# Optimization experiments

Measured on AMD Instinct MI355X. Metric: run time of the kernel, lower is better.

Reference implementation:

```python
import jax, jax.numpy as jnp
import numpy as np
import itertools

EPS = 1e-5
SCALE = 16 ** -0.5  # key_dim ** -0.5
H_HEADS, KEY_DIM, D, RES, RES_, STRIDE = 8, 16, 32, 28, 14, 2


def hardswish(x):
    return x * jnp.clip(x + 3.0, 0.0, 6.0) / 6.0


def conv_bn_hw(x, w, g, b, m, v):
    # 1x1 conv (no bias) + eval-mode BatchNorm + Hardswish
    y = jnp.einsum('bchw,oc->bohw', x, w)
    scale = (g / jnp.sqrt(v + EPS))[:, None, None]
    y = (y - m[:, None, None]) * scale + b[:, None, None]
    return hardswish(y)


def _bias_idxs():
    offsets, idxs = {}, []
    for p1 in itertools.product(range(RES_), repeat=2):
        for p2 in itertools.product(range(RES), repeat=2):
            off = (abs(p1[0] * STRIDE - p2[0]), abs(p1[1] * STRIDE - p2[1]))
            if off not in offsets:
                offsets[off] = len(offsets)
            idxs.append(offsets[off])
    return np.array(idxs, dtype=np.int32).reshape(RES_ * RES_, RES * RES), len(offsets)


def setup_inputs() -> dict:
    key = jax.random.key(0)
    ks = jax.random.split(key, 8)
    B, C = 64, 256
    idxs, n_off = _bias_idxs()

    def bn_params(k, n):
        k1, k2, k3, k4 = jax.random.split(k, 4)
        return (jax.random.normal(k1, (n,)) * 0.1 + 1.0,
                jax.random.normal(k2, (n,)) * 0.1,
                jax.random.normal(k3, (n,)) * 0.1,
                jax.random.uniform(k4, (n,), minval=0.5, maxval=1.5))

    kv_g, kv_b, kv_m, kv_v = bn_params(ks[1], 384)
    q_g, q_b, q_m, q_v = bn_params(ks[2], 128)
    p_g, p_b, p_m, p_v = bn_params(ks[3], 512)
    return dict(
        x=jax.random.normal(ks[0], (B, C, 28, 28), dtype=jnp.float32),
        kv_w=jax.random.normal(ks[4], (384, C)) * 0.05,
        kv_g=kv_g, kv_b=kv_b, kv_m=kv_m, kv_v=kv_v,
        q_w=jax.random.normal(ks[5], (128, C)) * 0.05,
        q_g=q_g, q_b=q_b, q_m=q_m, q_v=q_v,
        proj_w=jax.random.normal(ks[6], (512, 256)) * 0.05,
        proj_g=p_g, proj_b=p_b, proj_m=p_m, proj_v=p_v,
        ab=jax.random.normal(ks[7], (H_HEADS, n_off)) * 0.02,
        bias_idxs=jnp.asarray(idxs),
    )


def reference(x, kv_w, kv_g, kv_b, kv_m, kv_v, q_w, q_g, q_b, q_m, q_v,
              proj_w, proj_g, proj_b, proj_m, proj_v, ab, bias_idxs):
    B = x.shape[0]
    N, N_ = RES * RES, RES_ * RES_
    kv = conv_bn_hw(x, kv_w, kv_g, kv_b, kv_m, kv_v).reshape(B, H_HEADS, KEY_DIM + D, N)
    k, v = kv[:, :, :KEY_DIM], kv[:, :, KEY_DIM:]
    # AvgPool2d(kernel=1, stride=2) == strided slice
    q = conv_bn_hw(x[:, :, ::STRIDE, ::STRIDE], q_w, q_g, q_b, q_m, q_v)
    q = q.reshape(B, H_HEADS, KEY_DIM, N_)
    bias = ab[:, bias_idxs]  # gather -> [H, N_, N]
    attn = jax.nn.softmax(jnp.einsum('bhdn,bhdm->bhnm', q, k) * SCALE + bias, axis=-1)
    out = jnp.einsum('bhdm,bhnm->bhdn', v, attn).reshape(B, H_HEADS * D, RES_, RES_)
    return conv_bn_hw(hardswish(out), proj_w, proj_g, proj_b, proj_m, proj_v)
```

## Files before the change

### kernel.cpp

```cpp
#include <hip/hip_runtime.h>
#include <cstddef>


#define SCALE_ATTN 0.25f
#define BN_EPS 1e-5f

typedef short s8v  __attribute__((ext_vector_type(8)));
typedef short s4v  __attribute__((ext_vector_type(4)));
typedef float f4v  __attribute__((ext_vector_type(4)));

__device__ __forceinline__ float hswish(float y) {
    float t = fminf(fmaxf(y + 3.0f, 0.0f), 6.0f);
    return y * t * (1.0f / 6.0f);
}

__device__ __forceinline__ unsigned short bf16_rn(float f) {
    unsigned u = __float_as_uint(f);
    unsigned r = (u + 0x7FFFu + ((u >> 16) & 1u)) >> 16;
    return (unsigned short)r;
}
__device__ __forceinline__ float bf16_to_f(unsigned short h) {
    return __uint_as_float(((unsigned)h) << 16);
}

__global__ __launch_bounds__(256)
void bias_kernel(const float* __restrict__ ab, const int* __restrict__ idxs,
                 unsigned short* __restrict__ biasB, int n_off)
{
    __shared__ int I[32][33];
    int mx = blockIdx.x * 32, ny = blockIdx.y * 32;
    int tx = threadIdx.x & 31, ty = threadIdx.x >> 5;
#pragma unroll
    for (int i = 0; i < 4; ++i) {
        int nl = ty + i * 8;
        int n = ny + nl, m = mx + tx;
        I[tx][nl] = (n < 196 && m < 784) ? idxs[n * 784 + m] : 0;
    }
    __syncthreads();
#pragma unroll
    for (int i = 0; i < 4; ++i) {
        int ml = ty + i * 8;
        int m = mx + ml, n = ny + tx;
        if (m < 784 && n < 208) {
            float v = 0.0f;
            if (n < 196) {
                int id = I[ml][tx];
#pragma unroll
                for (int h = 0; h < 8; ++h) {
                    biasB[((size_t)h * 784 + m) * 208 + n] = bf16_rn(ab[h * n_off + id]);
                }
            } else {
#pragma unroll
                for (int h = 0; h < 8; ++h) {
                    biasB[((size_t)h * 784 + m) * 208 + n] = 0;
                }
            }
            (void)v;
        }
    }
}

template<bool STRIDED>
__global__ __launch_bounds__(256)
void convbn_mfma(const float* __restrict__ X, const float* __restrict__ W,
                 const float* __restrict__ G, const float* __restrict__ Bb,
                 const float* __restrict__ Mm, const float* __restrict__ Vv,
                 float* __restrict__ Y, int O, int N, int xbstride, int HWsrc)
{
    __shared__ short Ah[64][72];
    __shared__ short Al[64][72];
    __shared__ short Bh[64][72];
    __shared__ short Bl[64][72];
    __shared__ float scs[64], shs[64];

    const int C = 256;
    int b = blockIdx.z;
    int oBase = blockIdx.y * 64;
    int nBase = blockIdx.x * 64;
    const float* Xb = X + (size_t)b * xbstride;
    int tid = threadIdx.x;
    int w = tid >> 6, l = tid & 63;
    int wm = w >> 1, wn = w & 1;

    if (tid < 64) {
        int o = oBase + tid;
        float sc = G[o] * rsqrtf(Vv[o] + BN_EPS);
        scs[tid] = sc;
        shs[tid] = Bb[o] - Mm[o] * sc;
    }

    f4v acc[2][2];
#pragma unroll
    for (int i = 0; i < 2; ++i)
#pragma unroll
        for (int j = 0; j < 2; ++j) acc[i][j] = (f4v)0.0f;

    int sr  = tid >> 4;
    int sc4 = (tid & 15) * 4;
    int fr = l & 15, fk = (l >> 4) * 8;

    for (int c0 = 0; c0 < C; c0 += 64) {
        __syncthreads();
#pragma unroll
        for (int jo = 0; jo < 4; ++jo) {
            int o = sr + jo * 16;
            float4 wv = *reinterpret_cast<const float4*>(
                &W[(size_t)(oBase + o) * C + c0 + sc4]);
            s4v hv, lv;
            {
                unsigned short h;
                h = bf16_rn(wv.x); hv[0] = (short)h; lv[0] = (short)bf16_rn(wv.x - bf16_to_f(h));
                h = bf16_rn(wv.y); hv[1] = (short)h; lv[1] = (short)bf16_rn(wv.y - bf16_to_f(h));
                h = bf16_rn(wv.z); hv[2] = (short)h; lv[2] = (short)bf16_rn(wv.z - bf16_to_f(h));
                h = bf16_rn(wv.w); hv[3] = (short)h; lv[3] = (short)bf16_rn(wv.w - bf16_to_f(h));
            }
            *reinterpret_cast<s4v*>(&Ah[o][sc4]) = hv;
            *reinterpret_cast<s4v*>(&Al[o][sc4]) = lv;
        }
#pragma unroll
        for (int jc = 0; jc < 4; ++jc) {
            int c = sr + jc * 16;
            float vals[4];
            if (!STRIDED) {
                if (nBase + sc4 + 3 < N) {
                    float4 xv = *reinterpret_cast<const float4*>(
                        &Xb[(size_t)(c0 + c) * HWsrc + nBase + sc4]);
                    vals[0] = xv.x; vals[1] = xv.y; vals[2] = xv.z; vals[3] = xv.w;
                } else {
#pragma unroll
                    for (int e = 0; e < 4; ++e) {
                        int nn = nBase + sc4 + e;
                        vals[e] = (nn < N) ? Xb[(size_t)(c0 + c) * HWsrc + nn] : 0.0f;
                    }
                }
            } else {
#pragma unroll
                for (int e = 0; e < 4; ++e) {
                    int nn = nBase + sc4 + e;
                    float vv = 0.0f;
                    if (nn < N) {
                        int r = nn / 14, cc = nn - r * 14;
                        vv = Xb[(size_t)(c0 + c) * HWsrc + r * 56 + cc * 2];
                    }
                    vals[e] = vv;
                }
            }
#pragma unroll
            for (int e = 0; e < 4; ++e) {
                unsigned short h = bf16_rn(vals[e]);
                Bh[sc4 + e][c] = (short)h;
                Bl[sc4 + e][c] = (short)bf16_rn(vals[e] - bf16_to_f(h));
            }
        }
        __syncthreads();
#pragma unroll
        for (int ks = 0; ks < 2; ++ks) {
            s8v aH[2], aL[2], bH[2], bL[2];
#pragma unroll
            for (int mf = 0; mf < 2; ++mf) {
                aH[mf] = *reinterpret_cast<const s8v*>(&Ah[wm * 32 + mf * 16 + fr][ks * 32 + fk]);
                aL[mf] = *reinterpret_cast<const s8v*>(&Al[wm * 32 + mf * 16 + fr][ks * 32 + fk]);
            }
#pragma unroll
            for (int nf = 0; nf < 2; ++nf) {
                bH[nf] = *reinterpret_cast<const s8v*>(&Bh[wn * 32 + nf * 16 + fr][ks * 32 + fk]);
                bL[nf] = *reinterpret_cast<const s8v*>(&Bl[wn * 32 + nf * 16 + fr][ks * 32 + fk]);
            }
#pragma unroll
            for (int mf = 0; mf < 2; ++mf)
#pragma unroll
                for (int nf = 0; nf < 2; ++nf) {
                    acc[mf][nf] = __builtin_amdgcn_mfma_f32_16x16x32_bf16(aH[mf], bH[nf], acc[mf][nf], 0, 0, 0);
                    acc[mf][nf] = __builtin_amdgcn_mfma_f32_16x16x32_bf16(aH[mf], bL[nf], acc[mf][nf], 0, 0, 0);
                    acc[mf][nf] = __builtin_amdgcn_mfma_f32_16x16x32_bf16(aL[mf], bH[nf], acc[mf][nf], 0, 0, 0);
                }
        }
    }

    int lr = l >> 4;
#pragma unroll
    for (int mf = 0; mf < 2; ++mf)
#pragma unroll
        for (int nf = 0; nf < 2; ++nf) {
            int n = nBase + wn * 32 + nf * 16 + fr;
            if (n < N) {
#pragma unroll
                for (int i = 0; i < 4; ++i) {
                    int ol = wm * 32 + mf * 16 + lr * 4 + i;
                    float v = acc[mf][nf][i] * scs[ol] + shs[ol];
                    Y[((size_t)b * O + oBase + ol) * N + n] = hswish(v);
                }
            }
        }
}

__global__ __launch_bounds__(256)
void attn_mfma(const float* __restrict__ kv, const float* __restrict__ q,
               const unsigned short* __restrict__ biasB, float* __restrict__ act)
{
    __shared__ short Kh[64][24];
    __shared__ short Kl[64][24];
    __shared__ short Vs[32][72];
    __shared__ unsigned short Bia[64][208];
    __shared__ short Pl[4][16][72];

    int bh = blockIdx.x;
    int b = bh >> 3, h = bh & 7;
    const float* kvb = kv + ((size_t)b * 384 + h * 48) * 784;
    const float* qb  = q  + ((size_t)b * 128 + h * 16) * 196;
    const unsigned short* bB = biasB + (size_t)h * 784 * 208;

    int tid = threadIdx.x;
    int w = tid >> 6, l = tid & 63;
    int g = l >> 4, fr = l & 15;

    s8v qh[4], ql[4];
#pragma unroll
    for (int i = 0; i < 4; ++i) { qh[i] = (s8v)0; ql[i] = (s8v)0; }
#pragma unroll
    for (int i = 0; i < 4; ++i) {
        int tile = i * 4 + w;
        if (tile < 13 && g < 2) {
            int n = tile * 16 + fr;
            if (n < 196) {
#pragma unroll
                for (int j = 0; j < 8; ++j) {
                    int d = g * 8 + j;
                    float qv = qb[(size_t)d * 196 + n];
                    unsigned short hh = bf16_rn(qv);
                    qh[i][j] = (short)hh;
                    ql[i][j] = (short)bf16_rn(qv - bf16_to_f(hh));
                }
            }
        }
    }

    f4v Oa[4][2];
    float M[4], L[4];
#pragma unroll
    for (int i = 0; i < 4; ++i) {
        Oa[i][0] = (f4v)0.0f; Oa[i][1] = (f4v)0.0f;
        M[i] = -1e30f; L[i] = 0.0f;
    }

#pragma unroll 1
    for (int ch = 0; ch < 13; ++ch) {
        int m0 = ch * 64;
        int mlim = (784 - m0 < 64) ? (784 - m0) : 64;
        __syncthreads();
        {
            int d = tid >> 4, m4 = tid & 15;
            float4 kvv = make_float4(0.f, 0.f, 0.f, 0.f);
            if (m4 * 4 < mlim)
                kvv = *reinterpret_cast<const float4*>(&kvb[(size_t)d * 784 + m0 + m4 * 4]);
            float e0[4] = {kvv.x, kvv.y, kvv.z, kvv.w};
#pragma unroll
            for (int e = 0; e < 4; ++e) {
                unsigned short hh = bf16_rn(e0[e]);
                Kh[m4 * 4 + e][d] = (short)hh;
                Kl[m4 * 4 + e][d] = (short)bf16_rn(e0[e] - bf16_to_f(hh));
            }
        }
        {
            int d = tid >> 3, m8 = (tid & 7) * 8;
            float4 a = make_float4(0.f, 0.f, 0.f, 0.f), c4 = a;
            if (m8 < mlim) {
                a  = *reinterpret_cast<const float4*>(&kvb[(size_t)(16 + d) * 784 + m0 + m8]);
                c4 = *reinterpret_cast<const float4*>(&kvb[(size_t)(16 + d) * 784 + m0 + m8 + 4]);
            }
            s4v v0, v1;
            v0[0] = (short)bf16_rn(a.x);  v0[1] = (short)bf16_rn(a.y);
            v0[2] = (short)bf16_rn(a.z);  v0[3] = (short)bf16_rn(a.w);
            v1[0] = (short)bf16_rn(c4.x); v1[1] = (short)bf16_rn(c4.y);
            v1[2] = (short)bf16_rn(c4.z); v1[3] = (short)bf16_rn(c4.w);
            *reinterpret_cast<s4v*>(&Vs[d][m8])     = v0;
            *reinterpret_cast<s4v*>(&Vs[d][m8 + 4]) = v1;
        }
        {
            for (int it = tid; it < 64 * 26; it += 256) {
                int r = it / 26, cseg = it - r * 26;
                int4 vz = make_int4(0, 0, 0, 0);
                if (r < mlim)
                    vz = *reinterpret_cast<const int4*>(&bB[(size_t)(m0 + r) * 208 + cseg * 8]);
                *reinterpret_cast<int4*>(&Bia[r][cseg * 8]) = vz;
            }
        }
        __syncthreads();

#pragma unroll
        for (int i = 0; i < 4; ++i) {
            int tile = i * 4 + w;
            if (tile >= 13) continue;
            int n = tile * 16 + fr;

            float s[4][4];
#pragma unroll
            for (int sub = 0; sub < 4; ++sub) {
                s8v ah = (s8v)0, al = (s8v)0;
                if (g < 2) {
                    ah = *reinterpret_cast<const s8v*>(&Kh[sub * 16 + fr][g * 8]);
                    al = *reinterpret_cast<const s8v*>(&Kl[sub * 16 + fr][g * 8]);
                }
                f4v acc = (f4v)0.0f;
                acc = __builtin_amdgcn_mfma_f32_16x16x32_bf16(ah, qh[i], acc, 0, 0, 0);
                acc = __builtin_amdgcn_mfma_f32_16x16x32_bf16(ah, ql[i], acc, 0, 0, 0);
                acc = __builtin_amdgcn_mfma_f32_16x16x32_bf16(al, qh[i], acc, 0, 0, 0);
#pragma unroll
                for (int e = 0; e < 4; ++e) {
                    int mm = sub * 16 + g * 4 + e;
                    s[sub][e] = acc[e] * SCALE_ATTN + bf16_to_f(Bia[mm][n]);
                }
            }
            float mx = s[0][0];
#pragma unroll
            for (int sub = 0; sub < 4; ++sub)
#pragma unroll
                for (int e = 0; e < 4; ++e) mx = fmaxf(mx, s[sub][e]);
            mx = fmaxf(mx, __shfl_xor(mx, 16));
            mx = fmaxf(mx, __shfl_xor(mx, 32));
            if (__any(mx > M[i] + 8.0f)) {
                float Mn = fmaxf(M[i], mx);
                float corr = __expf(M[i] - Mn);
                L[i] *= corr;
#pragma unroll
                for (int e = 0; e < 4; ++e) { Oa[i][0][e] *= corr; Oa[i][1][e] *= corr; }
                M[i] = Mn;
            }
            float Ls = 0.0f;
#pragma unroll
            for (int sub = 0; sub < 4; ++sub) {
                float p[4];
#pragma unroll
                for (int e = 0; e < 4; ++e) {
                    int mm = sub * 16 + g * 4 + e;
                    float pv = __expf(s[sub][e] - M[i]);
                    p[e] = (mm < mlim) ? pv : 0.0f;
                    Ls += p[e];
                }
                unsigned w0 = (unsigned)bf16_rn(p[0]) | ((unsigned)bf16_rn(p[1]) << 16);
                unsigned w1 = (unsigned)bf16_rn(p[2]) | ((unsigned)bf16_rn(p[3]) << 16);
                int mbase = sub * 16 + g * 4;
                *reinterpret_cast<unsigned*>(&Pl[w][fr][mbase])     = w0;
                *reinterpret_cast<unsigned*>(&Pl[w][fr][mbase + 2]) = w1;
            }
            Ls += __shfl_xor(Ls, 16);
            Ls += __shfl_xor(Ls, 32);
            L[i] += Ls;
#pragma unroll
            for (int kc = 0; kc < 2; ++kc) {
                s8v pf = *reinterpret_cast<const s8v*>(&Pl[w][fr][kc * 32 + g * 8]);
                s8v v0 = *reinterpret_cast<const s8v*>(&Vs[fr][kc * 32 + g * 8]);
                s8v v1 = *reinterpret_cast<const s8v*>(&Vs[16 + fr][kc * 32 + g * 8]);
                Oa[i][0] = __builtin_amdgcn_mfma_f32_16x16x32_bf16(v0, pf, Oa[i][0], 0, 0, 0);
                Oa[i][1] = __builtin_amdgcn_mfma_f32_16x16x32_bf16(v1, pf, Oa[i][1], 0, 0, 0);
            }
        }
    }

#pragma unroll
    for (int i = 0; i < 4; ++i) {
        int tile = i * 4 + w;
        if (tile >= 13) continue;
        int n = tile * 16 + fr;
        if (n < 196) {
            float inv = 1.0f / L[i];
#pragma unroll
            for (int dt = 0; dt < 2; ++dt)
#pragma unroll
                for (int e = 0; e < 4; ++e) {
                    int d = dt * 16 + g * 4 + e;
                    float z = Oa[i][dt][e] * inv;
                    act[((size_t)b * 256 + h * 32 + d) * 196 + n] = hswish(z);
                }
        }
    }
}

extern "C" void kernel_launch(void* const* d_in, const int* in_sizes, int n_in,
                              void* d_out, int out_size, void* d_ws, size_t ws_size,
                              hipStream_t stream) {
    const float* x      = (const float*)d_in[0];
    const float* kv_w   = (const float*)d_in[1];
    const float* kv_g   = (const float*)d_in[2];
    const float* kv_b   = (const float*)d_in[3];
    const float* kv_m   = (const float*)d_in[4];
    const float* kv_v   = (const float*)d_in[5];
    const float* q_w    = (const float*)d_in[6];
    const float* q_g    = (const float*)d_in[7];
    const float* q_b    = (const float*)d_in[8];
    const float* q_m    = (const float*)d_in[9];
    const float* q_v    = (const float*)d_in[10];
    const float* proj_w = (const float*)d_in[11];
    const float* proj_g = (const float*)d_in[12];
    const float* proj_b = (const float*)d_in[13];
    const float* proj_m = (const float*)d_in[14];
    const float* proj_v = (const float*)d_in[15];
    const float* ab     = (const float*)d_in[16];
    const int*   idxs   = (const int*)d_in[17];
    float* out = (float*)d_out;

    int n_off = in_sizes[16] / 8;

    const size_t KV_ELEMS   = (size_t)64 * 384 * 784;
    const size_t Q_ELEMS    = (size_t)64 * 128 * 196;
    const size_t BIAS_SHORT = (size_t)8 * 784 * 208;
    float* kvbuf = (float*)d_ws;
    float* qbuf  = kvbuf + KV_ELEMS;
    unsigned short* biasB = (unsigned short*)(qbuf + Q_ELEMS);
    float* actb  = (float*)(biasB + BIAS_SHORT);

    {
        dim3 g(25, 7);
        bias_kernel<<<g, 256, 0, stream>>>(ab, idxs, biasB, n_off);
    }
    {
        dim3 g(13, 6, 64);
        convbn_mfma<false><<<g, 256, 0, stream>>>(x, kv_w, kv_g, kv_b, kv_m, kv_v,
                                                  kvbuf, 384, 784, 256 * 784, 784);
    }
    {
        dim3 g(4, 2, 64);
        convbn_mfma<true><<<g, 256, 0, stream>>>(x, q_w, q_g, q_b, q_m, q_v,
                                                 qbuf, 128, 196, 256 * 784, 784);
    }
    {
        attn_mfma<<<512, 256, 0, stream>>>(kvbuf, qbuf, biasB, actb);
    }
    {
        dim3 g(4, 8, 64);
        convbn_mfma<false><<<g, 256, 0, stream>>>(actb, proj_w, proj_g, proj_b, proj_m, proj_v,
                                                  out, 512, 196, 256 * 196, 196);
    }
}
```

Before: 396.9 us.

## Pre-split weights and inputs to bf16 hi/lo, swizzled tiles, restructure GEMMs and attention

Weights are split into bf16 hi/lo once in prep kernels instead of in every GEMM block. The input x is transposed into swizzled bf16 hi/lo tiles that later GEMMs load directly into LDS with global_load_lds. Intermediates K, Q, V and the attention output are now stored in bf16 (hi/lo where needed) in layouts the next stage consumes, which cuts fp32 traffic and per-block conversion work. The GEMMs use a 128-row output tile, and attention is relaunched with 512 threads and a new tile assignment. This adds several extra launches, and V is stored as single bf16, which may change accuracy.

```diff
diff --git a/kernel.cpp b/kernel.cpp
--- a/kernel.cpp
+++ b/kernel.cpp
@@ -1,19 +1,19 @@
 #include <hip/hip_runtime.h>
 #include <cstddef>
+#include <cstdint>
 
 
 #define SCALE_ATTN 0.25f
 #define BN_EPS 1e-5f
 
-typedef short s8v  __attribute__((ext_vector_type(8)));
-typedef short s4v  __attribute__((ext_vector_type(4)));
-typedef float f4v  __attribute__((ext_vector_type(4)));
+typedef short s8v __attribute__((ext_vector_type(8)));
+typedef short s4v __attribute__((ext_vector_type(4)));
+typedef float f4v __attribute__((ext_vector_type(4)));
 
 __device__ __forceinline__ float hswish(float y) {
     float t = fminf(fmaxf(y + 3.0f, 0.0f), 6.0f);
     return y * t * (1.0f / 6.0f);
 }
-
 __device__ __forceinline__ unsigned short bf16_rn(float f) {
     unsigned u = __float_as_uint(f);
     unsigned r = (u + 0x7FFFu + ((u >> 16) & 1u)) >> 16;
@@ -21,6 +21,79 @@
 }
 __device__ __forceinline__ float bf16_to_f(unsigned short h) {
     return __uint_as_float(((unsigned)h) << 16);
+}
+__device__ __forceinline__ void gload_lds16(const void* gsrc, void* ldsdst) {
+    __builtin_amdgcn_global_load_lds(
+        (const __attribute__((address_space(1))) unsigned int*)gsrc,
+        (__attribute__((address_space(3))) unsigned int*)ldsdst, 16, 0, 0);
+}
+
+__global__ __launch_bounds__(256)
+void wprep(const float* __restrict__ W, short* __restrict__ hi,
+           short* __restrict__ lo, int n4)
+{
+    int i = blockIdx.x * 256 + threadIdx.x;
+    int stride = gridDim.x * 256;
+    for (; i < n4; i += stride) {
+        float4 v = reinterpret_cast<const float4*>(W)[i];
+        s4v h, l;
+        unsigned short hh;
+        hh = bf16_rn(v.x); h[0] = (short)hh; l[0] = (short)bf16_rn(v.x - bf16_to_f(hh));
+        hh = bf16_rn(v.y); h[1] = (short)hh; l[1] = (short)bf16_rn(v.y - bf16_to_f(hh));
+        hh = bf16_rn(v.z); h[2] = (short)hh; l[2] = (short)bf16_rn(v.z - bf16_to_f(hh));
+        hh = bf16_rn(v.w); h[3] = (short)hh; l[3] = (short)bf16_rn(v.w - bf16_to_f(hh));
+        reinterpret_cast<s4v*>(hi)[i] = h;
+        reinterpret_cast<s4v*>(lo)[i] = l;
+    }
+}
+
+__global__ __launch_bounds__(256)
+void xprep(const float* __restrict__ x, short* __restrict__ xT)
+{
+    __shared__ float T[64][65];
+    int nt = blockIdx.x, b = blockIdx.y;
+    int n0 = nt * 64;
+    const float* xb = x + (size_t)b * 256 * 784;
+    int t = threadIdx.x;
+    int cr = t >> 2, s = t & 3;
+
+    for (int ct = 0; ct < 4; ++ct) {
+        __syncthreads();
+#pragma unroll
+        for (int qq = 0; qq < 4; ++qq) {
+            int n = n0 + s * 16 + qq * 4;
+            float4 v = make_float4(0.f, 0.f, 0.f, 0.f);
+            if (n + 3 < 784)
+                v = *reinterpret_cast<const float4*>(&xb[(size_t)(ct * 64 + cr) * 784 + n]);
+            *reinterpret_cast<float4*>(&T[cr][s * 16 + qq * 4]) = v;
+        }
+        __syncthreads();
+        int r = cr;
+        if (n0 + r < 784) {
+            size_t tb = ((((size_t)b * 13 + nt) * 4 + ct) << 13);
+            short* hiB = xT + tb;
+            short* loB = xT + tb + 4096;
+            s8v h0, h1, l0, l1;
+#pragma unroll
+            for (int j = 0; j < 8; ++j) {
+                float f = T[s * 16 + j][r];
+                unsigned short hh = bf16_rn(f);
+                h0[j] = (short)hh; l0[j] = (short)bf16_rn(f - bf16_to_f(hh));
+            }
+#pragma unroll
+            for (int j = 0; j < 8; ++j) {
+                float f = T[s * 16 + 8 + j][r];
+                unsigned short hh = bf16_rn(f);
+                h1[j] = (short)hh; l1[j] = (short)bf16_rn(f - bf16_to_f(hh));
+            }
+            int sw = (r & 7) << 3;
+            int base = r * 64;
+            *reinterpret_cast<s8v*>(&hiB[base + ((s * 16) ^ sw)]) = h0;
+            *reinterpret_cast<s8v*>(&hiB[base + ((s * 16 + 8) ^ sw)]) = h1;
+            *reinterpret_cast<s8v*>(&loB[base + ((s * 16) ^ sw)]) = l0;
+            *reinterpret_cast<s8v*>(&loB[base + ((s * 16 + 8) ^ sw)]) = l1;
+        }
+    }
 }
 
 __global__ __launch_bounds__(256)
@@ -42,203 +115,267 @@
         int ml = ty + i * 8;
         int m = mx + ml, n = ny + tx;
         if (m < 784 && n < 208) {
-            float v = 0.0f;
             if (n < 196) {
                 int id = I[ml][tx];
 #pragma unroll
-                for (int h = 0; h < 8; ++h) {
+                for (int h = 0; h < 8; ++h)
                     biasB[((size_t)h * 784 + m) * 208 + n] = bf16_rn(ab[h * n_off + id]);
-                }
             } else {
 #pragma unroll
-                for (int h = 0; h < 8; ++h) {
+                for (int h = 0; h < 8; ++h)
                     biasB[((size_t)h * 784 + m) * 208 + n] = 0;
-                }
-            }
-            (void)v;
-        }
-    }
-}
-
-template<bool STRIDED>
+            }
+        }
+    }
+}
+
 __global__ __launch_bounds__(256)
-void convbn_mfma(const float* __restrict__ X, const float* __restrict__ W,
-                 const float* __restrict__ G, const float* __restrict__ Bb,
-                 const float* __restrict__ Mm, const float* __restrict__ Vv,
-                 float* __restrict__ Y, int O, int N, int xbstride, int HWsrc)
+void gemm_kv(const short* __restrict__ xT,
+             const short* __restrict__ Whi, const short* __restrict__ Wlo,
+             const float* __restrict__ G, const float* __restrict__ Bb,
+             const float* __restrict__ Mm, const float* __restrict__ Vv,
+             short* __restrict__ Kthi, short* __restrict__ Ktlo,
+             short* __restrict__ Vbf)
 {
-    __shared__ short Ah[64][72];
-    __shared__ short Al[64][72];
-    __shared__ short Bh[64][72];
-    __shared__ short Bl[64][72];
-    __shared__ float scs[64], shs[64];
-
-    const int C = 256;
-    int b = blockIdx.z;
-    int oBase = blockIdx.y * 64;
-    int nBase = blockIdx.x * 64;
-    const float* Xb = X + (size_t)b * xbstride;
-    int tid = threadIdx.x;
-    int w = tid >> 6, l = tid & 63;
-    int wm = w >> 1, wn = w & 1;
-
-    if (tid < 64) {
+    __shared__ short Bt[2][64][64];
+    __shared__ float scs[128], shs[128];
+
+    int nt = blockIdx.x, oy = blockIdx.y, b = blockIdx.z;
+    int oBase = oy * 128;
+    int tid = threadIdx.x, w = tid >> 6, l = tid & 63;
+    int fr = l & 15, g = l >> 4;
+
+    if (tid < 128) {
         int o = oBase + tid;
         float sc = G[o] * rsqrtf(Vv[o] + BN_EPS);
-        scs[tid] = sc;
-        shs[tid] = Bb[o] - Mm[o] * sc;
-    }
-
-    f4v acc[2][2];
+        scs[tid] = sc; shs[tid] = Bb[o] - Mm[o] * sc;
+    }
+
+    f4v acc[2][4];
 #pragma unroll
     for (int i = 0; i < 2; ++i)
 #pragma unroll
-        for (int j = 0; j < 2; ++j) acc[i][j] = (f4v)0.0f;
-
-    int sr  = tid >> 4;
-    int sc4 = (tid & 15) * 4;
-    int fr = l & 15, fk = (l >> 4) * 8;
-
-    for (int c0 = 0; c0 < C; c0 += 64) {
-        __syncthreads();
-#pragma unroll
-        for (int jo = 0; jo < 4; ++jo) {
-            int o = sr + jo * 16;
-            float4 wv = *reinterpret_cast<const float4*>(
-                &W[(size_t)(oBase + o) * C + c0 + sc4]);
-            s4v hv, lv;
-            {
-                unsigned short h;
-                h = bf16_rn(wv.x); hv[0] = (short)h; lv[0] = (short)bf16_rn(wv.x - bf16_to_f(h));
-                h = bf16_rn(wv.y); hv[1] = (short)h; lv[1] = (short)bf16_rn(wv.y - bf16_to_f(h));
-                h = bf16_rn(wv.z); hv[2] = (short)h; lv[2] = (short)bf16_rn(wv.z - bf16_to_f(h));
-                h = bf16_rn(wv.w); hv[3] = (short)h; lv[3] = (short)bf16_rn(wv.w - bf16_to_f(h));
-            }
-            *reinterpret_cast<s4v*>(&Ah[o][sc4]) = hv;
-            *reinterpret_cast<s4v*>(&Al[o][sc4]) = lv;
-        }
+        for (int j = 0; j < 4; ++j) acc[i][j] = (f4v)0.0f;
+
+    const char* tilesrc = (const char*)(xT) + ((((size_t)b * 13 + nt) * 4) << 14);
+    char* ldsbase = (char*)&Bt[0][0][0];
+
+    for (int ct = 0; ct < 4; ++ct) {
+        __syncthreads();
+        {
+            const char* src = tilesrc + ((size_t)ct << 14) + w * 4096 + l * 16;
+            char* dst = ldsbase + w * 4096;
+#pragma unroll
+            for (int j = 0; j < 4; ++j)
+                gload_lds16(src + j * 1024, dst + j * 1024);
+        }
+        __syncthreads();
+#pragma unroll
+        for (int ks = 0; ks < 2; ++ks) {
+            s8v ah[2], al[2];
+#pragma unroll
+            for (int mf = 0; mf < 2; ++mf) {
+                int o = oBase + w * 32 + mf * 16 + fr;
+                size_t wi = (size_t)o * 256 + ct * 64 + ks * 32 + g * 8;
+                ah[mf] = *reinterpret_cast<const s8v*>(&Whi[wi]);
+                al[mf] = *reinterpret_cast<const s8v*>(&Wlo[wi]);
+            }
+#pragma unroll
+            for (int nf = 0; nf < 4; ++nf) {
+                int r = nf * 16 + fr;
+                int ci = (ks * 32 + g * 8) ^ ((r & 7) << 3);
+                s8v bh = *reinterpret_cast<const s8v*>(&Bt[0][r][ci]);
+                s8v bl = *reinterpret_cast<const s8v*>(&Bt[1][r][ci]);
+#pragma unroll
+                for (int mf = 0; mf < 2; ++mf) {
+                    acc[mf][nf] = __builtin_amdgcn_mfma_f32_16x16x32_bf16(ah[mf], bh, acc[mf][nf], 0, 0, 0);
+                    acc[mf][nf] = __builtin_amdgcn_mfma_f32_16x16x32_bf16(ah[mf], bl, acc[mf][nf], 0, 0, 0);
+                    acc[mf][nf] = __builtin_amdgcn_mfma_f32_16x16x32_bf16(al[mf], bh, acc[mf][nf], 0, 0, 0);
+                }
+            }
+        }
+    }
+
+    int nBase = nt * 64;
+#pragma unroll
+    for (int mf = 0; mf < 2; ++mf) {
+        int ol = w * 32 + mf * 16 + g * 4;
+        int o = oBase + ol;
+        int h = o / 48;
+        int c = o - h * 48;
+        if (c < 16) {
+#pragma unroll
+            for (int nf = 0; nf < 4; ++nf) {
+                int n = nBase + nf * 16 + fr;
+                if (n < 784) {
+                    s4v hv, lv;
+#pragma unroll
+                    for (int e = 0; e < 4; ++e) {
+                        float z = hswish(acc[mf][nf][e] * scs[ol + e] + shs[ol + e]);
+                        unsigned short hh = bf16_rn(z);
+                        hv[e] = (short)hh; lv[e] = (short)bf16_rn(z - bf16_to_f(hh));
+                    }
+                    size_t ki = (((size_t)b * 8 + h) * 784 + n) * 16 + c;
+                    *reinterpret_cast<s4v*>(&Kthi[ki]) = hv;
+                    *reinterpret_cast<s4v*>(&Ktlo[ki]) = lv;
+                }
+            }
+        } else {
+            int d = c - 16;
+#pragma unroll
+            for (int nf = 0; nf < 4; ++nf) {
+                int n = nBase + nf * 16 + fr;
+                if (n < 784) {
+#pragma unroll
+                    for (int e = 0; e < 4; ++e) {
+                        float z = hswish(acc[mf][nf][e] * scs[ol + e] + shs[ol + e]);
+                        Vbf[(((size_t)b * 8 + h) * 32 + d + e) * 784 + n] = (short)bf16_rn(z);
+                    }
+                }
+            }
+        }
+    }
+}
+
+__global__ __launch_bounds__(256)
+void gemm_q(const float* __restrict__ x,
+            const short* __restrict__ Whi, const short* __restrict__ Wlo,
+            const float* __restrict__ G, const float* __restrict__ Bb,
+            const float* __restrict__ Mm, const float* __restrict__ Vv,
+            short* __restrict__ Qthi, short* __restrict__ Qtlo)
+{
+    __shared__ short Bt[2][64][64];
+    __shared__ float scs[128], shs[128];
+
+    int nt = blockIdx.x, b = blockIdx.z;
+    const float* xb = x + (size_t)b * 256 * 784;
+    int tid = threadIdx.x, w = tid >> 6, l = tid & 63;
+    int fr = l & 15, g = l >> 4;
+    int sr = tid >> 4, sc4 = (tid & 15) * 4;
+
+    if (tid < 128) {
+        int o = tid;
+        float sc = G[o] * rsqrtf(Vv[o] + BN_EPS);
+        scs[tid] = sc; shs[tid] = Bb[o] - Mm[o] * sc;
+    }
+
+    f4v acc[2][4];
+#pragma unroll
+    for (int i = 0; i < 2; ++i)
+#pragma unroll
+        for (int j = 0; j < 4; ++j) acc[i][j] = (f4v)0.0f;
+
+    for (int ct = 0; ct < 4; ++ct) {
+        __syncthreads();
 #pragma unroll
         for (int jc = 0; jc < 4; ++jc) {
             int c = sr + jc * 16;
-            float vals[4];
-            if (!STRIDED) {
-                if (nBase + sc4 + 3 < N) {
-                    float4 xv = *reinterpret_cast<const float4*>(
-                        &Xb[(size_t)(c0 + c) * HWsrc + nBase + sc4]);
-                    vals[0] = xv.x; vals[1] = xv.y; vals[2] = xv.z; vals[3] = xv.w;
-                } else {
-#pragma unroll
-                    for (int e = 0; e < 4; ++e) {
-                        int nn = nBase + sc4 + e;
-                        vals[e] = (nn < N) ? Xb[(size_t)(c0 + c) * HWsrc + nn] : 0.0f;
-                    }
-                }
-            } else {
+#pragma unroll
+            for (int e = 0; e < 4; ++e) {
+                int nn = nt * 64 + sc4 + e;
+                float v = 0.0f;
+                if (nn < 196) {
+                    int rr = nn / 14, cc = nn - rr * 14;
+                    v = xb[(size_t)(ct * 64 + c) * 784 + rr * 56 + cc * 2];
+                }
+                int r = sc4 + e;
+                int ci = c ^ ((r & 7) << 3);
+                unsigned short hh = bf16_rn(v);
+                Bt[0][r][ci] = (short)hh;
+                Bt[1][r][ci] = (short)bf16_rn(v - bf16_to_f(hh));
+            }
+        }
+        __syncthreads();
+#pragma unroll
+        for (int ks = 0; ks < 2; ++ks) {
+            s8v ah[2], al[2];
+#pragma unroll
+            for (int mf = 0; mf < 2; ++mf) {
+                int o = w * 32 + mf * 16 + fr;
+                size_t wi = (size_t)o * 256 + ct * 64 + ks * 32 + g * 8;
+                ah[mf] = *reinterpret_cast<const s8v*>(&Whi[wi]);
+                al[mf] = *reinterpret_cast<const s8v*>(&Wlo[wi]);
+            }
+#pragma unroll
+            for (int nf = 0; nf < 4; ++nf) {
+                int r = nf * 16 + fr;
+                int ci = (ks * 32 + g * 8) ^ ((r & 7) << 3);
+                s8v bh = *reinterpret_cast<const s8v*>(&Bt[0][r][ci]);
+                s8v bl = *reinterpret_cast<const s8v*>(&Bt[1][r][ci]);
+#pragma unroll
+                for (int mf = 0; mf < 2; ++mf) {
+                    acc[mf][nf] = __builtin_amdgcn_mfma_f32_16x16x32_bf16(ah[mf], bh, acc[mf][nf], 0, 0, 0);
+                    acc[mf][nf] = __builtin_amdgcn_mfma_f32_16x16x32_bf16(ah[mf], bl, acc[mf][nf], 0, 0, 0);
+                    acc[mf][nf] = __builtin_amdgcn_mfma_f32_16x16x32_bf16(al[mf], bh, acc[mf][nf], 0, 0, 0);
+                }
+            }
+        }
+    }
+
+#pragma unroll
+    for (int mf = 0; mf < 2; ++mf) {
+        int ol = w * 32 + mf * 16 + g * 4;
+        int h = ol >> 4, d0 = ol & 15;
+#pragma unroll
+        for (int nf = 0; nf < 4; ++nf) {
+            int n = nt * 64 + nf * 16 + fr;
+            if (n < 196) {
+                s4v hv, lv;
 #pragma unroll
                 for (int e = 0; e < 4; ++e) {
-                    int nn = nBase + sc4 + e;
-                    float vv = 0.0f;
-                    if (nn < N) {
-                        int r = nn / 14, cc = nn - r * 14;
-                        vv = Xb[(size_t)(c0 + c) * HWsrc + r * 56 + cc * 2];
-                    }
-                    vals[e] = vv;
-                }
-            }
-#pragma unroll
-            for (int e = 0; e < 4; ++e) {
-                unsigned short h = bf16_rn(vals[e]);
-                Bh[sc4 + e][c] = (short)h;
-                Bl[sc4 + e][c] = (short)bf16_rn(vals[e] - bf16_to_f(h));
-            }
-        }
-        __syncthreads();
-#pragma unroll
-        for (int ks = 0; ks < 2; ++ks) {
-            s8v aH[2], aL[2], bH[2], bL[2];
-#pragma unroll
-            for (int mf = 0; mf < 2; ++mf) {
-                aH[mf] = *reinterpret_cast<const s8v*>(&Ah[wm * 32 + mf * 16 + fr][ks * 32 + fk]);
-                aL[mf] = *reinterpret_cast<const s8v*>(&Al[wm * 32 + mf * 16 + fr][ks * 32 + fk]);
-            }
-#pragma unroll
-            for (int nf = 0; nf < 2; ++nf) {
-                bH[nf] = *reinterpret_cast<const s8v*>(&Bh[wn * 32 + nf * 16 + fr][ks * 32 + fk]);
-                bL[nf] = *reinterpret_cast<const s8v*>(&Bl[wn * 32 + nf * 16 + fr][ks * 32 + fk]);
-            }
-#pragma unroll
-            for (int mf = 0; mf < 2; ++mf)
-#pragma unroll
-                for (int nf = 0; nf < 2; ++nf) {
-                    acc[mf][nf] = __builtin_amdgcn_mfma_f32_16x16x32_bf16(aH[mf], bH[nf], acc[mf][nf], 0, 0, 0);
-                    acc[mf][nf] = __builtin_amdgcn_mfma_f32_16x16x32_bf16(aH[mf], bL[nf], acc[mf][nf], 0, 0, 0);
-                    acc[mf][nf] = __builtin_amdgcn_mfma_f32_16x16x32_bf16(aL[mf], bH[nf], acc[mf][nf], 0, 0, 0);
-                }
-        }
-    }
-
-    int lr = l >> 4;
-#pragma unroll
-    for (int mf = 0; mf < 2; ++mf)
-#pragma unroll
-        for (int nf = 0; nf < 2; ++nf) {
-            int n = nBase + wn * 32 + nf * 16 + fr;
-            if (n < N) {
-#pragma unroll
-                for (int i = 0; i < 4; ++i) {
-                    int ol = wm * 32 + mf * 16 + lr * 4 + i;
-                    float v = acc[mf][nf][i] * scs[ol] + shs[ol];
-                    Y[((size_t)b * O + oBase + ol) * N + n] = hswish(v);
-                }
-            }
-        }
-}
-
-__global__ __launch_bounds__(256)
-void attn_mfma(const float* __restrict__ kv, const float* __restrict__ q,
-               const unsigned short* __restrict__ biasB, float* __restrict__ act)
+                    float z = hswish(acc[mf][nf][e] * scs[ol + e] + shs[ol + e]);
+                    unsigned short hh = bf16_rn(z);
+                    hv[e] = (short)hh; lv[e] = (short)bf16_rn(z - bf16_to_f(hh));
+                }
+                size_t qi = (((size_t)b * 8 + h) * 196 + n) * 16 + d0;
+                *reinterpret_cast<s4v*>(&Qthi[qi]) = hv;
+                *reinterpret_cast<s4v*>(&Qtlo[qi]) = lv;
+            }
+        }
+    }
+}
+
+__global__ __launch_bounds__(512)
+void attn_mfma(const short* __restrict__ Kthi, const short* __restrict__ Ktlo,
+               const short* __restrict__ Vbf,
+               const short* __restrict__ Qthi, const short* __restrict__ Qtlo,
+               const unsigned short* __restrict__ biasB, short* __restrict__ actT)
 {
-    __shared__ short Kh[64][24];
-    __shared__ short Kl[64][24];
-    __shared__ short Vs[32][72];
-    __shared__ unsigned short Bia[64][208];
-    __shared__ short Pl[4][16][72];
+    __shared__ short Pl[8][16][72];
 
     int bh = blockIdx.x;
     int b = bh >> 3, h = bh & 7;
-    const float* kvb = kv + ((size_t)b * 384 + h * 48) * 784;
-    const float* qb  = q  + ((size_t)b * 128 + h * 16) * 196;
+    const short* Kh = Kthi + (size_t)bh * 784 * 16;
+    const short* Kl = Ktlo + (size_t)bh * 784 * 16;
+    const short* Vb = Vbf + (size_t)bh * 32 * 784;
+    const short* Qh = Qthi + (size_t)bh * 196 * 16;
+    const short* Ql = Qtlo + (size_t)bh * 196 * 16;
     const unsigned short* bB = biasB + (size_t)h * 784 * 208;
 
-    int tid = threadIdx.x;
-    int w = tid >> 6, l = tid & 63;
+    int tid = threadIdx.x, w = tid >> 6, l = tid & 63;
     int g = l >> 4, fr = l & 15;
 
-    s8v qh[4], ql[4];
-#pragma unroll
-    for (int i = 0; i < 4; ++i) { qh[i] = (s8v)0; ql[i] = (s8v)0; }
-#pragma unroll
-    for (int i = 0; i < 4; ++i) {
-        int tile = i * 4 + w;
-        if (tile < 13 && g < 2) {
-            int n = tile * 16 + fr;
+    int ntc = (w < 5) ? 2 : 1;
+    int ntile[2] = { w, 8 + w };
+
+    s8v qh[2], ql[2];
+#pragma unroll
+    for (int i = 0; i < 2; ++i) { qh[i] = (s8v)0; ql[i] = (s8v)0; }
+#pragma unroll
+    for (int i = 0; i < 2; ++i) {
+        if (i < ntc && g < 2) {
+            int n = ntile[i] * 16 + fr;
             if (n < 196) {
-#pragma unroll
-                for (int j = 0; j < 8; ++j) {
-                    int d = g * 8 + j;
-                    float qv = qb[(size_t)d * 196 + n];
-                    unsigned short hh = bf16_rn(qv);
-                    qh[i][j] = (short)hh;
-                    ql[i][j] = (short)bf16_rn(qv - bf16_to_f(hh));
-                }
-            }
-        }
-    }
-
-    f4v Oa[4][2];
-    float M[4], L[4];
-#pragma unroll
-    for (int i = 0; i < 4; ++i) {
+                qh[i] = *reinterpret_cast<const s8v*>(&Qh[(size_t)n * 16 + g * 8]);
+                ql[i] = *reinterpret_cast<const s8v*>(&Ql[(size_t)n * 16 + g * 8]);
+            }
+        }
+    }
+
+    f4v Oa[2][2];
+    float M[2], L[2];
+#pragma unroll
+    for (int i = 0; i < 2; ++i) {
         Oa[i][0] = (f4v)0.0f; Oa[i][1] = (f4v)0.0f;
         M[i] = -1e30f; L[i] = 0.0f;
     }
@@ -246,71 +383,39 @@
 #pragma unroll 1
     for (int ch = 0; ch < 13; ++ch) {
         int m0 = ch * 64;
-        int mlim = (784 - m0 < 64) ? (784 - m0) : 64;
-        __syncthreads();
-        {
-            int d = tid >> 4, m4 = tid & 15;
-            float4 kvv = make_float4(0.f, 0.f, 0.f, 0.f);
-            if (m4 * 4 < mlim)
-                kvv = *reinterpret_cast<const float4*>(&kvb[(size_t)d * 784 + m0 + m4 * 4]);
-            float e0[4] = {kvv.x, kvv.y, kvv.z, kvv.w};
-#pragma unroll
-            for (int e = 0; e < 4; ++e) {
-                unsigned short hh = bf16_rn(e0[e]);
-                Kh[m4 * 4 + e][d] = (short)hh;
-                Kl[m4 * 4 + e][d] = (short)bf16_rn(e0[e] - bf16_to_f(hh));
-            }
-        }
-        {
-            int d = tid >> 3, m8 = (tid & 7) * 8;
-            float4 a = make_float4(0.f, 0.f, 0.f, 0.f), c4 = a;
-            if (m8 < mlim) {
-                a  = *reinterpret_cast<const float4*>(&kvb[(size_t)(16 + d) * 784 + m0 + m8]);
-                c4 = *reinterpret_cast<const float4*>(&kvb[(size_t)(16 + d) * 784 + m0 + m8 + 4]);
-            }
-            s4v v0, v1;
-            v0[0] = (short)bf16_rn(a.x);  v0[1] = (short)bf16_rn(a.y);
-            v0[2] = (short)bf16_rn(a.z);  v0[3] = (short)bf16_rn(a.w);
-            v1[0] = (short)bf16_rn(c4.x); v1[1] = (short)bf16_rn(c4.y);
-            v1[2] = (short)bf16_rn(c4.z); v1[3] = (short)bf16_rn(c4.w);
-            *reinterpret_cast<s4v*>(&Vs[d][m8])     = v0;
-            *reinterpret_cast<s4v*>(&Vs[d][m8 + 4]) = v1;
-        }
-        {
-            for (int it = tid; it < 64 * 26; it += 256) {
-                int r = it / 26, cseg = it - r * 26;
-                int4 vz = make_int4(0, 0, 0, 0);
-                if (r < mlim)
-                    vz = *reinterpret_cast<const int4*>(&bB[(size_t)(m0 + r) * 208 + cseg * 8]);
-                *reinterpret_cast<int4*>(&Bia[r][cseg * 8]) = vz;
-            }
-        }
-        __syncthreads();
-
-#pragma unroll
-        for (int i = 0; i < 4; ++i) {
-            int tile = i * 4 + w;
-            if (tile >= 13) continue;
-            int n = tile * 16 + fr;
+        int subLim = (ch == 12) ? 1 : 4;
+        int mlim = (ch == 12) ? 16 : 64;
+#pragma unroll 1
+        for (int i = 0; i < 2; ++i) {
+            if (i >= ntc) continue;
+            int n = ntile[i] * 16 + fr;
 
             float s[4][4];
 #pragma unroll
             for (int sub = 0; sub < 4; ++sub) {
-                s8v ah = (s8v)0, al = (s8v)0;
-                if (g < 2) {
-                    ah = *reinterpret_cast<const s8v*>(&Kh[sub * 16 + fr][g * 8]);
-                    al = *reinterpret_cast<const s8v*>(&Kl[sub * 16 + fr][g * 8]);
-                }
-                f4v acc = (f4v)0.0f;
-                acc = __builtin_amdgcn_mfma_f32_16x16x32_bf16(ah, qh[i], acc, 0, 0, 0);
-                acc = __builtin_amdgcn_mfma_f32_16x16x32_bf16(ah, ql[i], acc, 0, 0, 0);
-                acc = __builtin_amdgcn_mfma_f32_16x16x32_bf16(al, qh[i], acc, 0, 0, 0);
-#pragma unroll
-                for (int e = 0; e < 4; ++e) {
-                    int mm = sub * 16 + g * 4 + e;
-                    s[sub][e] = acc[e] * SCALE_ATTN + bf16_to_f(Bia[mm][n]);
-                }
-            }
+                if (sub < subLim) {
+                    int mg = m0 + sub * 16 + fr;
+                    s8v ah = (s8v)0, al = (s8v)0;
+                    if (g < 2) {
+                        ah = *reinterpret_cast<const s8v*>(&Kh[(size_t)mg * 16 + g * 8]);
+                        al = *reinterpret_cast<const s8v*>(&Kl[(size_t)mg * 16 + g * 8]);
+                    }
+                    f4v a = (f4v)0.0f;
+                    a = __builtin_amdgcn_mfma_f32_16x16x32_bf16(ah, qh[i], a, 0, 0, 0);
+                    a = __builtin_amdgcn_mfma_f32_16x16x32_bf16(ah, ql[i], a, 0, 0, 0);
+                    a = __builtin_amdgcn_mfma_f32_16x16x32_bf16(al, qh[i], a, 0, 0, 0);
+#pragma unroll
+                    for (int e = 0; e < 4; ++e) {
+                        int mm = m0 + sub * 16 + g * 4 + e;
+                        float bia = bf16_to_f(bB[(size_t)mm * 208 + n]);
+                        s[sub][e] = a[e] * SCALE_ATTN + bia;
+                    }
+                } else {
+#pragma unroll
+                    for (int e = 0; e < 4; ++e) s[sub][e] = -1e30f;
+                }
+            }
+
             float mx = s[0][0];
 #pragma unroll
             for (int sub = 0; sub < 4; ++sub)
@@ -326,31 +431,37 @@
                 for (int e = 0; e < 4; ++e) { Oa[i][0][e] *= corr; Oa[i][1][e] *= corr; }
                 M[i] = Mn;
             }
+
             float Ls = 0.0f;
 #pragma unroll
             for (int sub = 0; sub < 4; ++sub) {
                 float p[4];
 #pragma unroll
                 for (int e = 0; e < 4; ++e) {
-                    int mm = sub * 16 + g * 4 + e;
+                    int mml = sub * 16 + g * 4 + e;
                     float pv = __expf(s[sub][e] - M[i]);
-                    p[e] = (mm < mlim) ? pv : 0.0f;
+                    p[e] = (mml < mlim) ? pv : 0.0f;
                     Ls += p[e];
                 }
                 unsigned w0 = (unsigned)bf16_rn(p[0]) | ((unsigned)bf16_rn(p[1]) << 16);
                 unsigned w1 = (unsigned)bf16_rn(p[2]) | ((unsigned)bf16_rn(p[3]) << 16);
-                int mbase = sub * 16 + g * 4;
-                *reinterpret_cast<unsigned*>(&Pl[w][fr][mbase])     = w0;
-                *reinterpret_cast<unsigned*>(&Pl[w][fr][mbase + 2]) = w1;
+                int mb = sub * 16 + g * 4;
+                *reinterpret_cast<unsigned*>(&Pl[w][fr][mb]) = w0;
+                *reinterpret_cast<unsigned*>(&Pl[w][fr][mb + 2]) = w1;
             }
             Ls += __shfl_xor(Ls, 16);
             Ls += __shfl_xor(Ls, 32);
             L[i] += Ls;
+
 #pragma unroll
             for (int kc = 0; kc < 2; ++kc) {
                 s8v pf = *reinterpret_cast<const s8v*>(&Pl[w][fr][kc * 32 + g * 8]);
-                s8v v0 = *reinterpret_cast<const s8v*>(&Vs[fr][kc * 32 + g * 8]);
-                s8v v1 = *reinterpret_cast<const s8v*>(&Vs[16 + fr][kc * 32 + g * 8]);
+                int mf0 = m0 + kc * 32 + g * 8;
+                s8v v0 = (s8v)0, v1 = (s8v)0;
+                if (mf0 + 8 <= 784) {
+                    v0 = *reinterpret_cast<const s8v*>(&Vb[(size_t)fr * 784 + mf0]);
+                    v1 = *reinterpret_cast<const s8v*>(&Vb[(size_t)(16 + fr) * 784 + mf0]);
+                }
                 Oa[i][0] = __builtin_amdgcn_mfma_f32_16x16x32_bf16(v0, pf, Oa[i][0], 0, 0, 0);
                 Oa[i][1] = __builtin_amdgcn_mfma_f32_16x16x32_bf16(v1, pf, Oa[i][1], 0, 0, 0);
             }
@@ -358,20 +469,112 @@
     }
 
 #pragma unroll
-    for (int i = 0; i < 4; ++i) {
-        int tile = i * 4 + w;
-        if (tile >= 13) continue;
-        int n = tile * 16 + fr;
+    for (int i = 0; i < 2; ++i) {
+        if (i >= ntc) continue;
+        int n = ntile[i] * 16 + fr;
         if (n < 196) {
             float inv = 1.0f / L[i];
-#pragma unroll
-            for (int dt = 0; dt < 2; ++dt)
+            int r = n & 63, ntl = n >> 6;
+            int sw = (r & 7) << 3;
+#pragma unroll
+            for (int dt = 0; dt < 2; ++dt) {
+                int c0 = h * 32 + dt * 16 + g * 4;
+                s4v hv, lv;
 #pragma unroll
                 for (int e = 0; e < 4; ++e) {
-                    int d = dt * 16 + g * 4 + e;
-                    float z = Oa[i][dt][e] * inv;
-                    act[((size_t)b * 256 + h * 32 + d) * 196 + n] = hswish(z);
-                }
+                    float z = hswish(Oa[i][dt][e] * inv);
+                    unsigned short hh = bf16_rn(z);
+                    hv[e] = (short)hh; lv[e] = (short)bf16_rn(z - bf16_to_f(hh));
+                }
+                int ct = c0 >> 6, c2 = c0 & 63;
+                size_t tb = ((((size_t)b * 4 + ntl) * 4 + ct) << 13);
+                int idx = r * 64 + (c2 ^ sw);
+                *reinterpret_cast<s4v*>(&actT[tb + idx]) = hv;
+                *reinterpret_cast<s4v*>(&actT[tb + 4096 + idx]) = lv;
+            }
+        }
+    }
+}
+
+__global__ __launch_bounds__(256)
+void gemm_proj(const short* __restrict__ actT,
+               const short* __restrict__ Whi, const short* __restrict__ Wlo,
+               const float* __restrict__ G, const float* __restrict__ Bb,
+               const float* __restrict__ Mm, const float* __restrict__ Vv,
+               float* __restrict__ out)
+{
+    __shared__ short Bt[2][64][64];
+    __shared__ float scs[128], shs[128];
+
+    int nt = blockIdx.x, oy = blockIdx.y, b = blockIdx.z;
+    int oBase = oy * 128;
+    int tid = threadIdx.x, w = tid >> 6, l = tid & 63;
+    int fr = l & 15, g = l >> 4;
+
+    if (tid < 128) {
+        int o = oBase + tid;
+        float sc = G[o] * rsqrtf(Vv[o] + BN_EPS);
+        scs[tid] = sc; shs[tid] = Bb[o] - Mm[o] * sc;
+    }
+
+    f4v acc[2][4];
+#pragma unroll
+    for (int i = 0; i < 2; ++i)
+#pragma unroll
+        for (int j = 0; j < 4; ++j) acc[i][j] = (f4v)0.0f;
+
+    const char* tilesrc = (const char*)(actT) + ((((size_t)b * 4 + nt) * 4) << 14);
+    char* ldsbase = (char*)&Bt[0][0][0];
+
+    for (int ct = 0; ct < 4; ++ct) {
+        __syncthreads();
+        {
+            const char* src = tilesrc + ((size_t)ct << 14) + w * 4096 + l * 16;
+            char* dst = ldsbase + w * 4096;
+#pragma unroll
+            for (int j = 0; j < 4; ++j)
+                gload_lds16(src + j * 1024, dst + j * 1024);
+        }
+        __syncthreads();
+#pragma unroll
+        for (int ks = 0; ks < 2; ++ks) {
+            s8v ah[2], al[2];
+#pragma unroll
+            for (int mf = 0; mf < 2; ++mf) {
+                int o = oBase + w * 32 + mf * 16 + fr;
+                size_t wi = (size_t)o * 256 + ct * 64 + ks * 32 + g * 8;
+                ah[mf] = *reinterpret_cast<const s8v*>(&Whi[wi]);
+                al[mf] = *reinterpret_cast<const s8v*>(&Wlo[wi]);
+            }
+#pragma unroll
+            for (int nf = 0; nf < 4; ++nf) {
+                int r = nf * 16 + fr;
+                int ci = (ks * 32 + g * 8) ^ ((r & 7) << 3);
+                s8v bh = *reinterpret_cast<const s8v*>(&Bt[0][r][ci]);
+                s8v bl = *reinterpret_cast<const s8v*>(&Bt[1][r][ci]);
+#pragma unroll
+                for (int mf = 0; mf < 2; ++mf) {
+                    acc[mf][nf] = __builtin_amdgcn_mfma_f32_16x16x32_bf16(ah[mf], bh, acc[mf][nf], 0, 0, 0);
+                    acc[mf][nf] = __builtin_amdgcn_mfma_f32_16x16x32_bf16(ah[mf], bl, acc[mf][nf], 0, 0, 0);
+                    acc[mf][nf] = __builtin_amdgcn_mfma_f32_16x16x32_bf16(al[mf], bh, acc[mf][nf], 0, 0, 0);
+                }
+            }
+        }
+    }
+
+#pragma unroll
+    for (int mf = 0; mf < 2; ++mf) {
+        int ol = w * 32 + mf * 16 + g * 4;
+#pragma unroll
+        for (int nf = 0; nf < 4; ++nf) {
+            int n = nt * 64 + nf * 16 + fr;
+            if (n < 196) {
+#pragma unroll
+                for (int e = 0; e < 4; ++e) {
+                    float z = hswish(acc[mf][nf][e] * scs[ol + e] + shs[ol + e]);
+                    out[((size_t)b * 512 + oBase + ol + e) * 196 + n] = z;
+                }
+            }
         }
     }
 }
@@ -401,34 +604,38 @@
 
     int n_off = in_sizes[16] / 8;
 
-    const size_t KV_ELEMS   = (size_t)64 * 384 * 784;
-    const size_t Q_ELEMS    = (size_t)64 * 128 * 196;
-    const size_t BIAS_SHORT = (size_t)8 * 784 * 208;
-    float* kvbuf = (float*)d_ws;
-    float* qbuf  = kvbuf + KV_ELEMS;
-    unsigned short* biasB = (unsigned short*)(qbuf + Q_ELEMS);
-    float* actb  = (float*)(biasB + BIAS_SHORT);
-
-    {
-        dim3 g(25, 7);
-        bias_kernel<<<g, 256, 0, stream>>>(ab, idxs, biasB, n_off);
-    }
-    {
-        dim3 g(13, 6, 64);
-        convbn_mfma<false><<<g, 256, 0, stream>>>(x, kv_w, kv_g, kv_b, kv_m, kv_v,
-                                                  kvbuf, 384, 784, 256 * 784, 784);
-    }
-    {
-        dim3 g(4, 2, 64);
-        convbn_mfma<true><<<g, 256, 0, stream>>>(x, q_w, q_g, q_b, q_m, q_v,
-                                                 qbuf, 128, 196, 256 * 784, 784);
-    }
-    {
-        attn_mfma<<<512, 256, 0, stream>>>(kvbuf, qbuf, biasB, actb);
-    }
-    {
-        dim3 g(4, 8, 64);
-        convbn_mfma<false><<<g, 256, 0, stream>>>(actb, proj_w, proj_g, proj_b, proj_m, proj_v,
-                                                  out, 512, 196, 256 * 196, 196);
-    }
-}
+    char* p = (char*)d_ws;
+    size_t off = 0;
+    auto alloc = [&](size_t bytes) -> char* {
+        char* r = p + off;
+        off += (bytes + 255) & ~(size_t)255;
+        return r;
+    };
+    short* Kthi = (short*)alloc((size_t)64 * 8 * 784 * 16 * 2);
+    short* Ktlo = (short*)alloc((size_t)64 * 8 * 784 * 16 * 2);
+    short* Vbf  = (short*)alloc((size_t)64 * 8 * 32 * 784 * 2);
+    short* Qthi = (short*)alloc((size_t)64 * 8 * 196 * 16 * 2);
+    short* Qtlo = (short*)alloc((size_t)64 * 8 * 196 * 16 * 2);
+    unsigned short* biasB = (unsigned short*)alloc((size_t)8 * 784 * 208 * 2);
+    short* Wkvh = (short*)alloc((size_t)384 * 256 * 2);
+    short* Wkvl = (short*)alloc((size_t)384 * 256 * 2);
+    short* Wqh  = (short*)alloc((size_t)128 * 256 * 2);
+    short* Wql  = (short*)alloc((size_t)128 * 256 * 2);
+    short* Wpjh = (short*)alloc((size_t)512 * 256 * 2);
+    short* Wpjl = (short*)alloc((size_t)512 * 256 * 2);
+    short* xT   = (short*)alloc((size_t)64 * 13 * 4 * 16384);
+    short* actT = xT;
+
+    wprep<<<dim3(64), 256, 0, stream>>>(kv_w, Wkvh, Wkvl, 384 * 256 / 4);
+    wprep<<<dim3(64), 256, 0, stream>>>(q_w, Wqh, Wql, 128 * 256 / 4);
+    wprep<<<dim3(64), 256, 0, stream>>>(proj_w, Wpjh, Wpjl, 512 * 256 / 4);
+    xprep<<<dim3(13, 64), 256, 0, stream>>>(x, xT);
+    bias_kernel<<<dim3(25, 7), 256, 0, stream>>>(ab, idxs, biasB, n_off);
+    gemm_kv<<<dim3(13, 3, 64), 256, 0, stream>>>(xT, Wkvh, Wkvl, kv_g, kv_b, kv_m, kv_v,
+                                                 Kthi, Ktlo, Vbf);
+    gemm_q<<<dim3(4, 1, 64), 256, 0, stream>>>(x, Wqh, Wql, q_g, q_b, q_m, q_v,
+                                               Qthi, Qtlo);
+    attn_mfma<<<dim3(512), 512, 0, stream>>>(Kthi, Ktlo, Vbf, Qthi, Qtlo, biasB, actT);
+    gemm_proj<<<dim3(4, 4, 64), 256, 0, stream>>>(actT, Wpjh, Wpjl,
+                                                  proj_g, proj_b, proj_m, proj_v, out);
+}
```

New measurement: 449.5 us. 13.2% more time.
